# Kernel optimization log

Hardware: AMD Instinct MI355X
Metric: run time of the kernel (lower is better)

The kernel has to match this reference:

```python
import jax, jax.numpy as jnp
import numpy as np

EMBED_DIM = 256
SEQ_LEN = 4096
BATCH = 8
ALPHA = 0.99


def setup_inputs() -> dict:
    key = jax.random.key(0)
    k_x, k_w, k_b = jax.random.split(key, 3)
    x = jax.random.normal(k_x, (BATCH, SEQ_LEN, EMBED_DIM), dtype=jnp.float32)
    # nn.Linear(embed_dim, 3*embed_dim): store as [d, 3d] so y = x @ Wqkv + bqkv
    Wqkv = jax.random.normal(k_w, (EMBED_DIM, 3 * EMBED_DIM), dtype=jnp.float32) * (EMBED_DIM ** -0.5)
    bqkv = jax.random.normal(k_b, (3 * EMBED_DIM,), dtype=jnp.float32) * 0.02
    return {"x": x, "Wqkv": Wqkv, "bqkv": bqkv}


def reference(x, Wqkv, bqkv):
    bs, sl, d = x.shape
    qkv = x @ Wqkv + bqkv                      # [bs, sl, 3d]
    q, k, v = jnp.split(qkv, 3, axis=-1)       # each [bs, sl, d]
    # causal * exponential-decay mask: M[i, j] = alpha**(i-j) for j <= i else 0
    i = jnp.arange(sl, dtype=jnp.float32)
    M = jnp.where(i[:, None] >= i[None, :],
                  jnp.power(jnp.float32(ALPHA), i[:, None] - i[None, :]),
                  0.0)                          # [sl, sl]
    scores = jnp.einsum('bqd,bkd->bqk', q, k) / jnp.sqrt(jnp.float32(d))
    out = jnp.einsum('bqk,bkd->bqd', scores * M, v)
    return out
```

## Files before the change

kernel.cpp:

```cpp
#include <hip/hip_runtime.h>

typedef __bf16 bf16x8 __attribute__((ext_vector_type(8)));
typedef float f32x4 __attribute__((ext_vector_type(4)));
typedef unsigned short u16;
typedef unsigned int u32;
typedef u16 u16x4 __attribute__((ext_vector_type(4)));
typedef u16 u16x8 __attribute__((ext_vector_type(8)));

#define L2ALPHA (-0.014499569f)
#define WIN 1024

static __device__ __forceinline__ u16 f2bf(float f) {
    u32 u = __builtin_bit_cast(u32, f);
    return (u16)((u + 0x7FFFu + ((u >> 16) & 1u)) >> 16);
}

static __device__ __forceinline__ void gl2lds16(const void* g, void* l) {
    __builtin_amdgcn_global_load_lds(
        (const __attribute__((address_space(1))) u32*)g,
        (__attribute__((address_space(3))) u32*)l, 16, 0, 0);
}

__global__ __launch_bounds__(256, 2) void proj_kernel(
        const float* __restrict__ x, const float* __restrict__ Wq,
        const float* __restrict__ bias,
        u16* __restrict__ qb, u16* __restrict__ kb, u16* __restrict__ vb)
{
    __shared__ __align__(16) u16 Bs[32 * 128 * 8];
    __shared__ __align__(16) u16 As[4][32 * 40];

    const int tid = threadIdx.x, lane = tid & 63, w = tid >> 6;
    const int l = blockIdx.x;
    const int nb = l % 6;
    const int mt = l / 6;
    const int m0 = mt * 128, n0 = nb * 128;
    const int m = lane & 15, quad = lane >> 4;

    {
        const int col = tid & 127;
        const int khalf = tid >> 7;
        #pragma unroll
        for (int s = 0; s < 32; ++s) {
            int k0 = (khalf + 2 * s) * 4;
            u16x4 h;
            #pragma unroll
            for (int i = 0; i < 4; ++i)
                h[i] = f2bf(Wq[(k0 + i) * 768 + n0 + col]);
            *(u16x4*)&Bs[((k0 >> 3) * 128 + col) * 8 + (k0 & 7)] = h;
        }
    }
    __syncthreads();

    const int r = lane & 31, h = lane >> 5;
    const float* xrow = x + (size_t)(m0 + w * 32 + r) * 256 + h * 16;
    u16* As_w = &As[w][0];

    f32x4 acc[2][8];
    #pragma unroll
    for (int rt = 0; rt < 2; ++rt)
        #pragma unroll
        for (int ct = 0; ct < 8; ++ct)
            acc[rt][ct] = f32x4{0.f, 0.f, 0.f, 0.f};

    float4 g0 = *(const float4*)(xrow + 0);
    float4 g1 = *(const float4*)(xrow + 4);
    float4 g2 = *(const float4*)(xrow + 8);
    float4 g3 = *(const float4*)(xrow + 12);

    for (int kt = 0; kt < 8; ++kt) {
        u16x8 ha, hb;
        ha[0]=f2bf(g0.x); ha[1]=f2bf(g0.y); ha[2]=f2bf(g0.z); ha[3]=f2bf(g0.w);
        ha[4]=f2bf(g1.x); ha[5]=f2bf(g1.y); ha[6]=f2bf(g1.z); ha[7]=f2bf(g1.w);
        hb[0]=f2bf(g2.x); hb[1]=f2bf(g2.y); hb[2]=f2bf(g2.z); hb[3]=f2bf(g2.w);
        hb[4]=f2bf(g3.x); hb[5]=f2bf(g3.y); hb[6]=f2bf(g3.z); hb[7]=f2bf(g3.w);
        *(u16x8*)&As_w[r * 40 + h * 16]     = ha;
        *(u16x8*)&As_w[r * 40 + h * 16 + 8] = hb;

        if (kt < 7) {
            const float* xn = xrow + (kt + 1) * 32;
            g0 = *(const float4*)(xn + 0);
            g1 = *(const float4*)(xn + 4);
            g2 = *(const float4*)(xn + 8);
            g3 = *(const float4*)(xn + 12);
        }

        asm volatile("s_waitcnt lgkmcnt(0)" ::: "memory");

        bf16x8 af[2], bfr[8];
        #pragma unroll
        for (int rt = 0; rt < 2; ++rt)
            af[rt] = *(const bf16x8*)&As_w[(rt * 16 + m) * 40 + quad * 8];
        #pragma unroll
        for (int ct = 0; ct < 8; ++ct)
            bfr[ct] = *(const bf16x8*)&Bs[((kt * 4 + quad) * 128 + ct * 16 + m) * 8];
        #pragma unroll
        for (int rt = 0; rt < 2; ++rt)
            #pragma unroll
            for (int ct = 0; ct < 8; ++ct)
                acc[rt][ct] = __builtin_amdgcn_mfma_f32_16x16x32_bf16(
                    af[rt], bfr[ct], acc[rt][ct], 0, 0, 0);
    }

    const int b = m0 >> 12;
    const int jbase = (m0 & 4095) + w * 32;
    const int d0 = (nb & 1) * 128;

    if (nb < 2) {
        #pragma unroll
        for (int rt = 0; rt < 2; ++rt)
            #pragma unroll
            for (int ct = 0; ct < 8; ++ct) {
                int coll = ct * 16 + m;
                float bv = bias[d0 + coll];
                #pragma unroll
                for (int rr = 0; rr < 4; ++rr) {
                    int row = m0 + w * 32 + rt * 16 + quad * 4 + rr;
                    qb[(size_t)row * 256 + d0 + coll] = f2bf((acc[rt][ct][rr] + bv) * 0.0625f);
                }
            }
    } else if (nb < 4) {
        #pragma unroll
        for (int rt = 0; rt < 2; ++rt)
            #pragma unroll
            for (int ct = 0; ct < 8; ++ct) {
                int d = d0 + ct * 16 + m;
                float bv = bias[256 + d];
                int k8 = d >> 5, qk = (d >> 3) & 3, e = d & 7;
                #pragma unroll
                for (int rr = 0; rr < 4; ++rr) {
                    int j = jbase + rt * 16 + quad * 4 + rr;
                    int jt = j >> 5, jj = j & 31;
                    kb[((((size_t)(b * 128 + jt) * 2 + (jj & 1)) * 8 + k8) * 64 + qk * 16 + (jj >> 1)) * 8 + e]
                        = f2bf(acc[rt][ct][rr] + bv);
                }
            }
    } else {
        #pragma unroll
        for (int rt = 0; rt < 2; ++rt)
            #pragma unroll
            for (int ct = 0; ct < 8; ++ct) {
                int d = d0 + ct * 16 + m;
                float bv = bias[512 + d];
                int dt = d >> 4, mv = d & 15;
                int j = jbase + rt * 16 + quad * 4;
                int jt = j >> 5, qv = (j >> 3) & 3, e0 = j & 7;
                u16x4 hv;
                #pragma unroll
                for (int rr = 0; rr < 4; ++rr) hv[rr] = f2bf(acc[rt][ct][rr] + bv);
                *(u16x4*)&vb[(((size_t)(b * 128 + jt) * 16 + dt) * 64 + qv * 16 + mv) * 8 + e0] = hv;
            }
    }
}

__global__ __launch_bounds__(256, 1) void attn_kernel(
        const u16* __restrict__ qb, const u16* __restrict__ kb,
        const u16* __restrict__ vb, float* __restrict__ out)
{
    __shared__ __align__(16) u16 RB[4][16384];
    __shared__ __align__(16) u16 Ps[4 * 32 * 40];

    const int tid = threadIdx.x, lane = tid & 63, w = tid >> 6;
    const int l = blockIdx.x;
    const int b = l & 7;
    const int m0 = (l >> 3) * 128;
    const int qrow0 = m0 + w * 32;
    const int m = lane & 15, quad = lane >> 4;
    const size_t rowbase = (size_t)b * 4096;
    const size_t pbase = (size_t)b * 128;

    bf16x8 qf[2][8];
    #pragma unroll
    for (int rg = 0; rg < 2; ++rg)
        #pragma unroll
        for (int k8 = 0; k8 < 8; ++k8)
            qf[rg][k8] = *(const bf16x8*)(qb + (rowbase + qrow0 + rg * 16 + m) * 256 + k8 * 32 + quad * 8);
    asm volatile("s_waitcnt vmcnt(0)" ::: "memory");

    float Arow[2][4];
    #pragma unroll
    for (int rg = 0; rg < 2; ++rg)
        #pragma unroll
        for (int rr = 0; rr < 4; ++rr)
            Arow[rg][rr] = __builtin_amdgcn_exp2f((float)(rg * 16 + quad * 4 + rr) * L2ALPHA);
    const float Em0 = __builtin_amdgcn_exp2f((float)(-2 * m) * L2ALPHA);
    const float Em1 = __builtin_amdgcn_exp2f((float)(-2 * m - 1) * L2ALPHA);

    f32x4 acc[2][16];
    #pragma unroll
    for (int rg = 0; rg < 2; ++rg)
        #pragma unroll
        for (int dt = 0; dt < 16; ++dt)
            acc[rg][dt] = f32x4{0.f, 0.f, 0.f, 0.f};

    int t0 = (m0 - WIN) >> 5; if (t0 < 0) t0 = 0;
    const int t1 = (m0 >> 5) + 3;
    const int nT = t1 - t0 + 1;

    #define STAGE(ix)                                                       \
        do {                                                                \
            const int buf_ = (ix) & 3;                                      \
            const u16* kp_ = kb + (pbase + t0 + (ix)) * 8192;               \
            const u16* vp_ = vb + (pbase + t0 + (ix)) * 8192;               \
            _Pragma("unroll")                                               \
            for (int s_ = 0; s_ < 4; ++s_) {                                \
                int c_ = tid + 256 * s_;                       \
                gl2lds16(kp_ + (size_t)c_ * 8, &RB[buf_][c_ * 8]);          \
                gl2lds16(vp_ + (size_t)c_ * 8, &RB[buf_][8192 + c_ * 8]);   \
            }                                                               \
        } while (0)

    STAGE(0); STAGE(1); STAGE(2);

    for (int it = 0; it < nT; ++it) {
        if (it <= nT - 3)      asm volatile("s_waitcnt vmcnt(16)" ::: "memory");
        else if (it == nT - 2) asm volatile("s_waitcnt vmcnt(8)" ::: "memory");
        else                   asm volatile("s_waitcnt vmcnt(0)" ::: "memory");
        __builtin_amdgcn_s_barrier();
        asm volatile("" ::: "memory");

        if (it + 3 < nT) STAGE(it + 3);

        const int t = t0 + it;
        const int j0 = t * 32;
        if (j0 <= qrow0 + 31 && j0 + (WIN + 31) >= qrow0) {
            const u16* Kt = &RB[it & 3][0];
            const u16* Vt = &RB[it & 3][8192];

            const float base = __builtin_amdgcn_exp2f((float)(qrow0 - j0) * L2ALPHA);
            const float C0 = base * Em0, C1 = base * Em1;
            const bool diag = (j0 == qrow0);

            f32x4 sA0{0.f,0.f,0.f,0.f}, sA1{0.f,0.f,0.f,0.f};
            f32x4 sB0{0.f,0.f,0.f,0.f}, sB1{0.f,0.f,0.f,0.f};
            #pragma unroll
            for (int k8 = 0; k8 < 8; ++k8) {
                bf16x8 bf0 = *(const bf16x8*)&Kt[(k8 * 64 + lane) * 8];
                sA0 = __builtin_amdgcn_mfma_f32_16x16x32_bf16(qf[0][k8], bf0, sA0, 0, 0, 0);
                sA1 = __builtin_amdgcn_mfma_f32_16x16x32_bf16(qf[1][k8], bf0, sA1, 0, 0, 0);
            }
            #pragma unroll
            for (int k8 = 0; k8 < 8; ++k8) {
                bf16x8 bf1 = *(const bf16x8*)&Kt[((8 + k8) * 64 + lane) * 8];
                sB0 = __builtin_amdgcn_mfma_f32_16x16x32_bf16(qf[0][k8], bf1, sB0, 0, 0, 0);
                sB1 = __builtin_amdgcn_mfma_f32_16x16x32_bf16(qf[1][k8], bf1, sB1, 0, 0, 0);
            }

            if (diag) {
                #pragma unroll
                for (int rg = 0; rg < 2; ++rg) {
                    f32x4 sh0 = rg ? sA1 : sA0;
                    f32x4 sh1 = rg ? sB1 : sB0;
                    #pragma unroll
                    for (int rr = 0; rr < 4; ++rr) {
                        int ioff = rg * 16 + quad * 4 + rr;
                        int dd0 = ioff - 2 * m;
                        float w0 = (dd0 >= 0) ? Arow[rg][rr] * C0 : 0.0f;
                        float w1 = (dd0 >= 1) ? Arow[rg][rr] * C1 : 0.0f;
                        u32 pv = (u32)f2bf(sh0[rr] * w0) | ((u32)f2bf(sh1[rr] * w1) << 16);
                        *(u32*)&Ps[(w * 32 + ioff) * 40 + 2 * m] = pv;
                    }
                }
            } else {
                #pragma unroll
                for (int rg = 0; rg < 2; ++rg) {
                    f32x4 sh0 = rg ? sA1 : sA0;
                    f32x4 sh1 = rg ? sB1 : sB0;
                    #pragma unroll
                    for (int rr = 0; rr < 4; ++rr) {
                        int ioff = rg * 16 + quad * 4 + rr;
                        float w0 = Arow[rg][rr] * C0;
                        float w1 = Arow[rg][rr] * C1;
                        u32 pv = (u32)f2bf(sh0[rr] * w0) | ((u32)f2bf(sh1[rr] * w1) << 16);
                        *(u32*)&Ps[(w * 32 + ioff) * 40 + 2 * m] = pv;
                    }
                }
            }
            asm volatile("s_waitcnt lgkmcnt(0)" ::: "memory");

            bf16x8 pa0 = *(const bf16x8*)&Ps[(w * 32 + m) * 40 + quad * 8];
            bf16x8 pa1 = *(const bf16x8*)&Ps[(w * 32 + 16 + m) * 40 + quad * 8];

            #pragma unroll
            for (int dt = 0; dt < 16; ++dt) {
                bf16x8 vf = *(const bf16x8*)&Vt[(dt * 64 + lane) * 8];
                acc[0][dt] = __builtin_amdgcn_mfma_f32_16x16x32_bf16(pa0, vf, acc[0][dt], 0, 0, 0);
                acc[1][dt] = __builtin_amdgcn_mfma_f32_16x16x32_bf16(pa1, vf, acc[1][dt], 0, 0, 0);
            }
        }
    }

    #pragma unroll
    for (int rg = 0; rg < 2; ++rg)
        #pragma unroll
        for (int dt = 0; dt < 16; ++dt)
            #pragma unroll
            for (int rr = 0; rr < 4; ++rr)
                out[(rowbase + qrow0 + rg * 16 + quad * 4 + rr) * 256 + dt * 16 + m] = acc[rg][dt][rr];
}

extern "C" void kernel_launch(void* const* d_in, const int* in_sizes, int n_in,
                              void* d_out, int out_size, void* d_ws, size_t ws_size,
                              hipStream_t stream) {
    (void)in_sizes; (void)n_in; (void)out_size; (void)ws_size;
    const float* x    = (const float*)d_in[0];
    const float* Wq   = (const float*)d_in[1];
    const float* bias = (const float*)d_in[2];
    float* outp = (float*)d_out;

    const size_t per = (size_t)8 * 4096 * 256;
    u16* qb = (u16*)d_ws;
    u16* kb = qb + per;
    u16* vb = kb + per;

    proj_kernel<<<1536, 256, 0, stream>>>(x, Wq, bias, qb, kb, vb);
    attn_kernel<<<256, 256, 0, stream>>>(qb, kb, vb, outp);
}
```

Before: 193.1 us.

## Split attention work across two wave groups per query tile

The attention kernel now launches 512 threads per block. Each query tile is shared by two waves: one handles the even key columns and half of the output dimensions, the other the odd key columns and the other half. The K/V ring shrinks from four stages to three so two blocks can share a CU, and s_setprio is placed around the MFMA loops. The aim is more waves per CU to hide latency and fewer accumulator registers per wave. In exchange the score-to-PV handoff needs an extra barrier and P is written to LDS as scattered 16-bit stores.

```diff
diff --git a/kernel.cpp b/kernel.cpp
--- a/kernel.cpp
+++ b/kernel.cpp
@@ -42,11 +42,11 @@
         #pragma unroll
         for (int s = 0; s < 32; ++s) {
             int k0 = (khalf + 2 * s) * 4;
-            u16x4 h;
+            u16x4 hh;
             #pragma unroll
             for (int i = 0; i < 4; ++i)
-                h[i] = f2bf(Wq[(k0 + i) * 768 + n0 + col]);
-            *(u16x4*)&Bs[((k0 >> 3) * 128 + col) * 8 + (k0 & 7)] = h;
+                hh[i] = f2bf(Wq[(k0 + i) * 768 + n0 + col]);
+            *(u16x4*)&Bs[((k0 >> 3) * 128 + col) * 8 + (k0 & 7)] = hh;
         }
     }
     __syncthreads();
@@ -152,18 +152,19 @@
     }
 }
 
-__global__ __launch_bounds__(256, 1) void attn_kernel(
+__global__ __launch_bounds__(512, 2) void attn_kernel(
         const u16* __restrict__ qb, const u16* __restrict__ kb,
         const u16* __restrict__ vb, float* __restrict__ out)
 {
-    __shared__ __align__(16) u16 RB[4][16384];
+    __shared__ __align__(16) u16 RB[3][16384];
     __shared__ __align__(16) u16 Ps[4 * 32 * 40];
 
     const int tid = threadIdx.x, lane = tid & 63, w = tid >> 6;
+    const int g = w & 3, h = w >> 2;
     const int l = blockIdx.x;
     const int b = l & 7;
     const int m0 = (l >> 3) * 128;
-    const int qrow0 = m0 + w * 32;
+    const int qrow0 = m0 + g * 32;
     const int m = lane & 15, quad = lane >> 4;
     const size_t rowbase = (size_t)b * 4096;
     const size_t pbase = (size_t)b * 128;
@@ -182,15 +183,14 @@
         #pragma unroll
         for (int rr = 0; rr < 4; ++rr)
             Arow[rg][rr] = __builtin_amdgcn_exp2f((float)(rg * 16 + quad * 4 + rr) * L2ALPHA);
-    const float Em0 = __builtin_amdgcn_exp2f((float)(-2 * m) * L2ALPHA);
-    const float Em1 = __builtin_amdgcn_exp2f((float)(-2 * m - 1) * L2ALPHA);
-
-    f32x4 acc[2][16];
+    const float Em = __builtin_amdgcn_exp2f((float)(-2 * m - h) * L2ALPHA);
+
+    f32x4 acc[2][8];
     #pragma unroll
     for (int rg = 0; rg < 2; ++rg)
         #pragma unroll
-        for (int dt = 0; dt < 16; ++dt)
-            acc[rg][dt] = f32x4{0.f, 0.f, 0.f, 0.f};
+        for (int dtl = 0; dtl < 8; ++dtl)
+            acc[rg][dtl] = f32x4{0.f, 0.f, 0.f, 0.f};
 
     int t0 = (m0 - WIN) >> 5; if (t0 < 0) t0 = 0;
     const int t1 = (m0 >> 5) + 3;
@@ -198,104 +198,101 @@
 
     #define STAGE(ix)                                                       \
         do {                                                                \
-            const int buf_ = (ix) & 3;                                      \
+            const int buf_ = (ix) % 3;                                      \
             const u16* kp_ = kb + (pbase + t0 + (ix)) * 8192;               \
             const u16* vp_ = vb + (pbase + t0 + (ix)) * 8192;               \
             _Pragma("unroll")                                               \
-            for (int s_ = 0; s_ < 4; ++s_) {                                \
-                int c_ = tid + 256 * s_;                       \
+            for (int s_ = 0; s_ < 2; ++s_) {                                \
+                int c_ = tid + 512 * s_;                       \
                 gl2lds16(kp_ + (size_t)c_ * 8, &RB[buf_][c_ * 8]);          \
                 gl2lds16(vp_ + (size_t)c_ * 8, &RB[buf_][8192 + c_ * 8]);   \
             }                                                               \
         } while (0)
 
-    STAGE(0); STAGE(1); STAGE(2);
+    STAGE(0); STAGE(1);
 
     for (int it = 0; it < nT; ++it) {
-        if (it <= nT - 3)      asm volatile("s_waitcnt vmcnt(16)" ::: "memory");
-        else if (it == nT - 2) asm volatile("s_waitcnt vmcnt(8)" ::: "memory");
-        else                   asm volatile("s_waitcnt vmcnt(0)" ::: "memory");
+        if (it + 1 < nT) asm volatile("s_waitcnt vmcnt(4)" ::: "memory");
+        else             asm volatile("s_waitcnt vmcnt(0)" ::: "memory");
         __builtin_amdgcn_s_barrier();
         asm volatile("" ::: "memory");
 
-        if (it + 3 < nT) STAGE(it + 3);
+        if (it + 2 < nT) STAGE(it + 2);
 
         const int t = t0 + it;
         const int j0 = t * 32;
-        if (j0 <= qrow0 + 31 && j0 + (WIN + 31) >= qrow0) {
-            const u16* Kt = &RB[it & 3][0];
-            const u16* Vt = &RB[it & 3][8192];
+        const bool valid = (j0 <= qrow0 + 31) && (j0 + (WIN + 31) >= qrow0);
+
+        if (valid) {
+            const u16* Kt = &RB[it % 3][0];
 
             const float base = __builtin_amdgcn_exp2f((float)(qrow0 - j0) * L2ALPHA);
-            const float C0 = base * Em0, C1 = base * Em1;
+            const float C = base * Em;
             const bool diag = (j0 == qrow0);
 
-            f32x4 sA0{0.f,0.f,0.f,0.f}, sA1{0.f,0.f,0.f,0.f};
-            f32x4 sB0{0.f,0.f,0.f,0.f}, sB1{0.f,0.f,0.f,0.f};
+            __builtin_amdgcn_s_setprio(1);
+            f32x4 s0{0.f,0.f,0.f,0.f}, s1{0.f,0.f,0.f,0.f};
             #pragma unroll
             for (int k8 = 0; k8 < 8; ++k8) {
-                bf16x8 bf0 = *(const bf16x8*)&Kt[(k8 * 64 + lane) * 8];
-                sA0 = __builtin_amdgcn_mfma_f32_16x16x32_bf16(qf[0][k8], bf0, sA0, 0, 0, 0);
-                sA1 = __builtin_amdgcn_mfma_f32_16x16x32_bf16(qf[1][k8], bf0, sA1, 0, 0, 0);
-            }
-            #pragma unroll
-            for (int k8 = 0; k8 < 8; ++k8) {
-                bf16x8 bf1 = *(const bf16x8*)&Kt[((8 + k8) * 64 + lane) * 8];
-                sB0 = __builtin_amdgcn_mfma_f32_16x16x32_bf16(qf[0][k8], bf1, sB0, 0, 0, 0);
-                sB1 = __builtin_amdgcn_mfma_f32_16x16x32_bf16(qf[1][k8], bf1, sB1, 0, 0, 0);
-            }
+                bf16x8 bf0 = *(const bf16x8*)&Kt[((h * 8 + k8) * 64 + lane) * 8];
+                s0 = __builtin_amdgcn_mfma_f32_16x16x32_bf16(qf[0][k8], bf0, s0, 0, 0, 0);
+                s1 = __builtin_amdgcn_mfma_f32_16x16x32_bf16(qf[1][k8], bf0, s1, 0, 0, 0);
+            }
+            __builtin_amdgcn_s_setprio(0);
 
             if (diag) {
                 #pragma unroll
                 for (int rg = 0; rg < 2; ++rg) {
-                    f32x4 sh0 = rg ? sA1 : sA0;
-                    f32x4 sh1 = rg ? sB1 : sB0;
+                    f32x4 sh = rg ? s1 : s0;
                     #pragma unroll
                     for (int rr = 0; rr < 4; ++rr) {
                         int ioff = rg * 16 + quad * 4 + rr;
-                        int dd0 = ioff - 2 * m;
-                        float w0 = (dd0 >= 0) ? Arow[rg][rr] * C0 : 0.0f;
-                        float w1 = (dd0 >= 1) ? Arow[rg][rr] * C1 : 0.0f;
-                        u32 pv = (u32)f2bf(sh0[rr] * w0) | ((u32)f2bf(sh1[rr] * w1) << 16);
-                        *(u32*)&Ps[(w * 32 + ioff) * 40 + 2 * m] = pv;
+                        int dd = ioff - 2 * m - h;
+                        float wgt = (dd >= 0) ? Arow[rg][rr] * C : 0.0f;
+                        Ps[(g * 32 + ioff) * 40 + 2 * m + h] = f2bf(sh[rr] * wgt);
                     }
                 }
             } else {
                 #pragma unroll
                 for (int rg = 0; rg < 2; ++rg) {
-                    f32x4 sh0 = rg ? sA1 : sA0;
-                    f32x4 sh1 = rg ? sB1 : sB0;
+                    f32x4 sh = rg ? s1 : s0;
                     #pragma unroll
                     for (int rr = 0; rr < 4; ++rr) {
                         int ioff = rg * 16 + quad * 4 + rr;
-                        float w0 = Arow[rg][rr] * C0;
-                        float w1 = Arow[rg][rr] * C1;
-                        u32 pv = (u32)f2bf(sh0[rr] * w0) | ((u32)f2bf(sh1[rr] * w1) << 16);
-                        *(u32*)&Ps[(w * 32 + ioff) * 40 + 2 * m] = pv;
+                        float wgt = Arow[rg][rr] * C;
+                        Ps[(g * 32 + ioff) * 40 + 2 * m + h] = f2bf(sh[rr] * wgt);
                     }
                 }
             }
-            asm volatile("s_waitcnt lgkmcnt(0)" ::: "memory");
-
-            bf16x8 pa0 = *(const bf16x8*)&Ps[(w * 32 + m) * 40 + quad * 8];
-            bf16x8 pa1 = *(const bf16x8*)&Ps[(w * 32 + 16 + m) * 40 + quad * 8];
-
-            #pragma unroll
-            for (int dt = 0; dt < 16; ++dt) {
-                bf16x8 vf = *(const bf16x8*)&Vt[(dt * 64 + lane) * 8];
-                acc[0][dt] = __builtin_amdgcn_mfma_f32_16x16x32_bf16(pa0, vf, acc[0][dt], 0, 0, 0);
-                acc[1][dt] = __builtin_amdgcn_mfma_f32_16x16x32_bf16(pa1, vf, acc[1][dt], 0, 0, 0);
-            }
+        }
+        asm volatile("s_waitcnt lgkmcnt(0)" ::: "memory");
+        __builtin_amdgcn_s_barrier();
+        asm volatile("" ::: "memory");
+
+        if (valid) {
+            const u16* Vt = &RB[it % 3][8192];
+            bf16x8 pa0 = *(const bf16x8*)&Ps[(g * 32 + m) * 40 + quad * 8];
+            bf16x8 pa1 = *(const bf16x8*)&Ps[(g * 32 + 16 + m) * 40 + quad * 8];
+
+            __builtin_amdgcn_s_setprio(1);
+            #pragma unroll
+            for (int dtl = 0; dtl < 8; ++dtl) {
+                bf16x8 vf = *(const bf16x8*)&Vt[((h * 8 + dtl) * 64 + lane) * 8];
+                acc[0][dtl] = __builtin_amdgcn_mfma_f32_16x16x32_bf16(pa0, vf, acc[0][dtl], 0, 0, 0);
+                acc[1][dtl] = __builtin_amdgcn_mfma_f32_16x16x32_bf16(pa1, vf, acc[1][dtl], 0, 0, 0);
+            }
+            __builtin_amdgcn_s_setprio(0);
         }
     }
 
     #pragma unroll
     for (int rg = 0; rg < 2; ++rg)
         #pragma unroll
-        for (int dt = 0; dt < 16; ++dt)
+        for (int dtl = 0; dtl < 8; ++dtl)
             #pragma unroll
             for (int rr = 0; rr < 4; ++rr)
-                out[(rowbase + qrow0 + rg * 16 + quad * 4 + rr) * 256 + dt * 16 + m] = acc[rg][dt][rr];
+                out[(rowbase + qrow0 + rg * 16 + quad * 4 + rr) * 256 + (h * 8 + dtl) * 16 + m]
+                    = acc[rg][dtl][rr];
 }
 
 extern "C" void kernel_launch(void* const* d_in, const int* in_sizes, int n_in,
@@ -313,5 +310,5 @@
     u16* vb = kb + per;
 
     proj_kernel<<<1536, 256, 0, stream>>>(x, Wq, bias, qb, kb, vb);
-    attn_kernel<<<256, 256, 0, stream>>>(qb, kb, vb, outp);
-}
+    attn_kernel<<<256, 512, 0, stream>>>(qb, kb, vb, outp);
+}
```

New measurement: 182.4 us. 5.6% less time.

## Warp-specialize attention into QK and PV wave groups with pipelined P buffers

Applied to the files above, without the earlier changes.

The attention kernel now runs 512 threads: four waves compute QK^T scores and write decayed P tiles into a double-buffered LDS area, while four other waves consume the previous tile's P with V, one iteration behind. K and V staging are split into separate rings with different prefetch depths, and s_setprio is raised around the MFMA bursts. The aim is to overlap the score computation and the PV accumulation across different waves so the matrix units stay busier. In exchange the block uses more LDS, adds an extra pipeline iteration, and the QK waves hold Q fragments while the PV waves hold the accumulators, which changes register pressure and occupancy.

```diff
diff --git a/kernel.cpp b/kernel.cpp
--- a/kernel.cpp
+++ b/kernel.cpp
@@ -42,11 +42,11 @@
         #pragma unroll
         for (int s = 0; s < 32; ++s) {
             int k0 = (khalf + 2 * s) * 4;
-            u16x4 h;
+            u16x4 hh;
             #pragma unroll
             for (int i = 0; i < 4; ++i)
-                h[i] = f2bf(Wq[(k0 + i) * 768 + n0 + col]);
-            *(u16x4*)&Bs[((k0 >> 3) * 128 + col) * 8 + (k0 & 7)] = h;
+                hh[i] = f2bf(Wq[(k0 + i) * 768 + n0 + col]);
+            *(u16x4*)&Bs[((k0 >> 3) * 128 + col) * 8 + (k0 & 7)] = hh;
         }
     }
     __syncthreads();
@@ -152,28 +152,33 @@
     }
 }
 
-__global__ __launch_bounds__(256, 1) void attn_kernel(
+__global__ __launch_bounds__(512, 2) void attn_kernel(
         const u16* __restrict__ qb, const u16* __restrict__ kb,
         const u16* __restrict__ vb, float* __restrict__ out)
 {
-    __shared__ __align__(16) u16 RB[4][16384];
-    __shared__ __align__(16) u16 Ps[4 * 32 * 40];
+    __shared__ __align__(16) u16 KR[4][8192];
+    __shared__ __align__(16) u16 VR[4][8192];
+    __shared__ __align__(16) u16 Ps[2][128 * 40];
 
     const int tid = threadIdx.x, lane = tid & 63, w = tid >> 6;
+    const int g = w & 3;
+    const bool isQK = (w < 4);
     const int l = blockIdx.x;
     const int b = l & 7;
     const int m0 = (l >> 3) * 128;
-    const int qrow0 = m0 + w * 32;
+    const int qrow0 = m0 + g * 32;
     const int m = lane & 15, quad = lane >> 4;
     const size_t rowbase = (size_t)b * 4096;
     const size_t pbase = (size_t)b * 128;
 
     bf16x8 qf[2][8];
-    #pragma unroll
-    for (int rg = 0; rg < 2; ++rg)
-        #pragma unroll
-        for (int k8 = 0; k8 < 8; ++k8)
-            qf[rg][k8] = *(const bf16x8*)(qb + (rowbase + qrow0 + rg * 16 + m) * 256 + k8 * 32 + quad * 8);
+    if (isQK) {
+        #pragma unroll
+        for (int rg = 0; rg < 2; ++rg)
+            #pragma unroll
+            for (int k8 = 0; k8 < 8; ++k8)
+                qf[rg][k8] = *(const bf16x8*)(qb + (rowbase + qrow0 + rg * 16 + m) * 256 + k8 * 32 + quad * 8);
+    }
     asm volatile("s_waitcnt vmcnt(0)" ::: "memory");
 
     float Arow[2][4];
@@ -196,106 +201,130 @@
     const int t1 = (m0 >> 5) + 3;
     const int nT = t1 - t0 + 1;
 
-    #define STAGE(ix)                                                       \
+    #define STAGE_K(ix)                                                     \
         do {                                                                \
-            const int buf_ = (ix) & 3;                                      \
             const u16* kp_ = kb + (pbase + t0 + (ix)) * 8192;               \
+            _Pragma("unroll")                                               \
+            for (int s_ = 0; s_ < 2; ++s_) {                                \
+                int c_ = tid + 512 * s_;                       \
+                gl2lds16(kp_ + (size_t)c_ * 8, &KR[(ix) & 3][c_ * 8]);      \
+            }                                                               \
+        } while (0)
+    #define STAGE_V(ix)                                                     \
+        do {                                                                \
             const u16* vp_ = vb + (pbase + t0 + (ix)) * 8192;               \
             _Pragma("unroll")                                               \
-            for (int s_ = 0; s_ < 4; ++s_) {                                \
-                int c_ = tid + 256 * s_;                       \
-                gl2lds16(kp_ + (size_t)c_ * 8, &RB[buf_][c_ * 8]);          \
-                gl2lds16(vp_ + (size_t)c_ * 8, &RB[buf_][8192 + c_ * 8]);   \
+            for (int s_ = 0; s_ < 2; ++s_) {                                \
+                int c_ = tid + 512 * s_;                                    \
+                gl2lds16(vp_ + (size_t)c_ * 8, &VR[(ix) & 3][c_ * 8]);      \
             }                                                               \
         } while (0)
 
-    STAGE(0); STAGE(1); STAGE(2);
-
-    for (int it = 0; it < nT; ++it) {
-        if (it <= nT - 3)      asm volatile("s_waitcnt vmcnt(16)" ::: "memory");
-        else if (it == nT - 2) asm volatile("s_waitcnt vmcnt(8)" ::: "memory");
+    STAGE_K(0); STAGE_K(1); STAGE_V(0); STAGE_K(2); STAGE_V(1);
+
+    for (int it = 0; it <= nT; ++it) {
+        if (it <= nT - 3)      asm volatile("s_waitcnt vmcnt(8)" ::: "memory");
+        else if (it == nT - 2) asm volatile("s_waitcnt vmcnt(6)" ::: "memory");
+        else if (it == nT - 1) asm volatile("s_waitcnt vmcnt(2)" ::: "memory");
         else                   asm volatile("s_waitcnt vmcnt(0)" ::: "memory");
         __builtin_amdgcn_s_barrier();
         asm volatile("" ::: "memory");
 
-        if (it + 3 < nT) STAGE(it + 3);
-
-        const int t = t0 + it;
-        const int j0 = t * 32;
-        if (j0 <= qrow0 + 31 && j0 + (WIN + 31) >= qrow0) {
-            const u16* Kt = &RB[it & 3][0];
-            const u16* Vt = &RB[it & 3][8192];
-
-            const float base = __builtin_amdgcn_exp2f((float)(qrow0 - j0) * L2ALPHA);
-            const float C0 = base * Em0, C1 = base * Em1;
-            const bool diag = (j0 == qrow0);
-
-            f32x4 sA0{0.f,0.f,0.f,0.f}, sA1{0.f,0.f,0.f,0.f};
-            f32x4 sB0{0.f,0.f,0.f,0.f}, sB1{0.f,0.f,0.f,0.f};
-            #pragma unroll
-            for (int k8 = 0; k8 < 8; ++k8) {
-                bf16x8 bf0 = *(const bf16x8*)&Kt[(k8 * 64 + lane) * 8];
-                sA0 = __builtin_amdgcn_mfma_f32_16x16x32_bf16(qf[0][k8], bf0, sA0, 0, 0, 0);
-                sA1 = __builtin_amdgcn_mfma_f32_16x16x32_bf16(qf[1][k8], bf0, sA1, 0, 0, 0);
-            }
-            #pragma unroll
-            for (int k8 = 0; k8 < 8; ++k8) {
-                bf16x8 bf1 = *(const bf16x8*)&Kt[((8 + k8) * 64 + lane) * 8];
-                sB0 = __builtin_amdgcn_mfma_f32_16x16x32_bf16(qf[0][k8], bf1, sB0, 0, 0, 0);
-                sB1 = __builtin_amdgcn_mfma_f32_16x16x32_bf16(qf[1][k8], bf1, sB1, 0, 0, 0);
-            }
-
-            if (diag) {
-                #pragma unroll
-                for (int rg = 0; rg < 2; ++rg) {
-                    f32x4 sh0 = rg ? sA1 : sA0;
-                    f32x4 sh1 = rg ? sB1 : sB0;
+        if (it + 3 < nT) STAGE_K(it + 3);
+        if (it + 2 < nT) STAGE_V(it + 2);
+
+        if (isQK) {
+            if (it < nT) {
+                const int j0 = (t0 + it) * 32;
+                if (j0 <= qrow0 + 31 && j0 + (WIN + 31) >= qrow0) {
+                    const u16* Kt = &KR[it & 3][0];
+                    const float base = __builtin_amdgcn_exp2f((float)(qrow0 - j0) * L2ALPHA);
+                    const float C0 = base * Em0, C1 = base * Em1;
+                    const bool diag = (j0 == qrow0);
+
+                    __builtin_amdgcn_s_setprio(1);
+                    f32x4 sA0{0.f,0.f,0.f,0.f}, sA1{0.f,0.f,0.f,0.f};
+                    f32x4 sB0{0.f,0.f,0.f,0.f}, sB1{0.f,0.f,0.f,0.f};
                     #pragma unroll
-                    for (int rr = 0; rr < 4; ++rr) {
-                        int ioff = rg * 16 + quad * 4 + rr;
-                        int dd0 = ioff - 2 * m;
-                        float w0 = (dd0 >= 0) ? Arow[rg][rr] * C0 : 0.0f;
-                        float w1 = (dd0 >= 1) ? Arow[rg][rr] * C1 : 0.0f;
-                        u32 pv = (u32)f2bf(sh0[rr] * w0) | ((u32)f2bf(sh1[rr] * w1) << 16);
-                        *(u32*)&Ps[(w * 32 + ioff) * 40 + 2 * m] = pv;
+                    for (int k8 = 0; k8 < 8; ++k8) {
+                        bf16x8 bf0 = *(const bf16x8*)&Kt[(k8 * 64 + lane) * 8];
+                        sA0 = __builtin_amdgcn_mfma_f32_16x16x32_bf16(qf[0][k8], bf0, sA0, 0, 0, 0);
+                        sA1 = __builtin_amdgcn_mfma_f32_16x16x32_bf16(qf[1][k8], bf0, sA1, 0, 0, 0);
+                    }
+                    #pragma unroll
+                    for (int k8 = 0; k8 < 8; ++k8) {
+                        bf16x8 bf1 = *(const bf16x8*)&Kt[((8 + k8) * 64 + lane) * 8];
+                        sB0 = __builtin_amdgcn_mfma_f32_16x16x32_bf16(qf[0][k8], bf1, sB0, 0, 0, 0);
+                        sB1 = __builtin_amdgcn_mfma_f32_16x16x32_bf16(qf[1][k8], bf1, sB1, 0, 0, 0);
+                    }
+                    __builtin_amdgcn_s_setprio(0);
+
+                    u16* Pw = &Ps[it & 1][0];
+                    if (diag) {
+                        #pragma unroll
+                        for (int rg = 0; rg < 2; ++rg) {
+                            f32x4 sh0 = rg ? sA1 : sA0;
+                            f32x4 sh1 = rg ? sB1 : sB0;
+                            #pragma unroll
+                            for (int rr = 0; rr < 4; ++rr) {
+                                int ioff = rg * 16 + quad * 4 + rr;
+                                int dd0 = ioff - 2 * m;
+                                float w0 = (dd0 >= 0) ? Arow[rg][rr] * C0 : 0.0f;
+                                float w1 = (dd0 >= 1) ? Arow[rg][rr] * C1 : 0.0f;
+                                u32 pv = (u32)f2bf(sh0[rr] * w0) | ((u32)f2bf(sh1[rr] * w1) << 16);
+                                *(u32*)&Pw[(g * 32 + ioff) * 40 + 2 * m] = pv;
+                            }
+                        }
+                    } else {
+                        #pragma unroll
+                        for (int rg = 0; rg < 2; ++rg) {
+                            f32x4 sh0 = rg ? sA1 : sA0;
+                            f32x4 sh1 = rg ? sB1 : sB0;
+                            #pragma unroll
+                            for (int rr = 0; rr < 4; ++rr) {
+                                int ioff = rg * 16 + quad * 4 + rr;
+                                float w0 = Arow[rg][rr] * C0;
+                                float w1 = Arow[rg][rr] * C1;
+                                u32 pv = (u32)f2bf(sh0[rr] * w0) | ((u32)f2bf(sh1[rr] * w1) << 16);
+                                *(u32*)&Pw[(g * 32 + ioff) * 40 + 2 * m] = pv;
+                            }
+                        }
                     }
                 }
-            } else {
+            }
+        } else {
+            if (it >= 1) {
+                const int j0 = (t0 + it - 1) * 32;
+                if (j0 <= qrow0 + 31 && j0 + (WIN + 31) >= qrow0) {
+                    const u16* Vt = &VR[(it - 1) & 3][0];
+                    const u16* Pr = &Ps[(it - 1) & 1][0];
+                    bf16x8 pa0 = *(const bf16x8*)&Pr[(g * 32 + m) * 40 + quad * 8];
+                    bf16x8 pa1 = *(const bf16x8*)&Pr[(g * 32 + 16 + m) * 40 + quad * 8];
+
+                    __builtin_amdgcn_s_setprio(1);
+                    #pragma unroll
+                    for (int dt = 0; dt < 16; ++dt) {
+                        bf16x8 vf = *(const bf16x8*)&Vt[(dt * 64 + lane) * 8];
+                        acc[0][dt] = __builtin_amdgcn_mfma_f32_16x16x32_bf16(pa0, vf, acc[0][dt], 0, 0, 0);
+                        acc[1][dt] = __builtin_amdgcn_mfma_f32_16x16x32_bf16(pa1, vf, acc[1][dt], 0, 0, 0);
+                    }
+                    __builtin_amdgcn_s_setprio(0);
+                }
+            }
+        }
+        asm volatile("s_waitcnt lgkmcnt(0)" ::: "memory");
+    }
+
+    if (!isQK) {
+        #pragma unroll
+        for (int rg = 0; rg < 2; ++rg)
+            #pragma unroll
+            for (int dt = 0; dt < 16; ++dt)
                 #pragma unroll
-                for (int rg = 0; rg < 2; ++rg) {
-                    f32x4 sh0 = rg ? sA1 : sA0;
-                    f32x4 sh1 = rg ? sB1 : sB0;
-                    #pragma unroll
-                    for (int rr = 0; rr < 4; ++rr) {
-                        int ioff = rg * 16 + quad * 4 + rr;
-                        float w0 = Arow[rg][rr] * C0;
-                        float w1 = Arow[rg][rr] * C1;
-                        u32 pv = (u32)f2bf(sh0[rr] * w0) | ((u32)f2bf(sh1[rr] * w1) << 16);
-                        *(u32*)&Ps[(w * 32 + ioff) * 40 + 2 * m] = pv;
-                    }
-                }
-            }
-            asm volatile("s_waitcnt lgkmcnt(0)" ::: "memory");
-
-            bf16x8 pa0 = *(const bf16x8*)&Ps[(w * 32 + m) * 40 + quad * 8];
-            bf16x8 pa1 = *(const bf16x8*)&Ps[(w * 32 + 16 + m) * 40 + quad * 8];
-
-            #pragma unroll
-            for (int dt = 0; dt < 16; ++dt) {
-                bf16x8 vf = *(const bf16x8*)&Vt[(dt * 64 + lane) * 8];
-                acc[0][dt] = __builtin_amdgcn_mfma_f32_16x16x32_bf16(pa0, vf, acc[0][dt], 0, 0, 0);
-                acc[1][dt] = __builtin_amdgcn_mfma_f32_16x16x32_bf16(pa1, vf, acc[1][dt], 0, 0, 0);
-            }
-        }
-    }
-
-    #pragma unroll
-    for (int rg = 0; rg < 2; ++rg)
-        #pragma unroll
-        for (int dt = 0; dt < 16; ++dt)
-            #pragma unroll
-            for (int rr = 0; rr < 4; ++rr)
-                out[(rowbase + qrow0 + rg * 16 + quad * 4 + rr) * 256 + dt * 16 + m] = acc[rg][dt][rr];
+                for (int rr = 0; rr < 4; ++rr)
+                    out[(rowbase + qrow0 + rg * 16 + quad * 4 + rr) * 256 + dt * 16 + m]
+                        = acc[rg][dt][rr];
+    }
 }
 
 extern "C" void kernel_launch(void* const* d_in, const int* in_sizes, int n_in,
@@ -313,5 +342,5 @@
     u16* vb = kb + per;
 
     proj_kernel<<<1536, 256, 0, stream>>>(x, Wq, bias, qb, kb, vb);
-    attn_kernel<<<256, 256, 0, stream>>>(qb, kb, vb, outp);
-}
+    attn_kernel<<<256, 512, 0, stream>>>(qb, kb, vb, outp);
+}
```

New measurement: 178.0 us. 7.9% less time.
